# Kernel optimization log

Hardware: AMD Instinct MI355X
Metric: run time of the kernel (lower is better)

Reference implementation:

```python
import jax, jax.numpy as jnp
import numpy as np

DIM = 256
HEADS = 8
W = 64  # window size (1D)
CPB = 512


def setup_inputs() -> dict:
    key = jax.random.key(0)
    ks = jax.random.split(key, 8)
    x = jax.random.normal(ks[0], (4096, W, DIM), dtype=jnp.float32)
    qkv_w = jax.random.normal(ks[1], (3 * DIM, DIM), dtype=jnp.float32) * (1.0 / np.sqrt(DIM))
    q_bias = jnp.zeros((DIM,), dtype=jnp.float32)
    v_bias = jnp.zeros((DIM,), dtype=jnp.float32)
    logit_scale = jnp.full((HEADS, 1, 1), np.log(10.0), dtype=jnp.float32)
    cpb_w1 = jax.random.normal(ks[2], (CPB, 1), dtype=jnp.float32)
    cpb_b1 = jnp.zeros((CPB,), dtype=jnp.float32)
    cpb_w2 = jax.random.normal(ks[3], (HEADS, CPB), dtype=jnp.float32) * (1.0 / np.sqrt(CPB))
    proj_w = jax.random.normal(ks[4], (DIM, DIM), dtype=jnp.float32) * (1.0 / np.sqrt(DIM))
    proj_b = jnp.zeros((DIM,), dtype=jnp.float32)
    return {"x": x, "qkv_w": qkv_w, "q_bias": q_bias, "v_bias": v_bias,
            "logit_scale": logit_scale, "cpb_w1": cpb_w1, "cpb_b1": cpb_b1,
            "cpb_w2": cpb_w2, "proj_w": proj_w, "proj_b": proj_b}


def _rel_coords_table():
    # [2W-1, 1] log-spaced continuous relative coordinates (Swin-v2 CPB input)
    t = jnp.arange(-(W - 1), W, dtype=jnp.float32) / (W - 1) * 8.0
    t = jnp.sign(t) * jnp.log2(jnp.abs(t) + 1.0) / np.log2(8.0)
    return t[:, None]


def _rel_index():
    c = jnp.arange(W)
    return c[:, None] - c[None, :] + (W - 1)  # [W, W] in [0, 2W-2]


def reference(x, qkv_w, q_bias, v_bias, logit_scale, cpb_w1, cpb_b1, cpb_w2, proj_w, proj_b):
    B_, N, C = x.shape
    hd = C // HEADS
    qkv_bias = jnp.concatenate([q_bias, jnp.zeros_like(v_bias), v_bias])
    qkv = x @ qkv_w.T + qkv_bias                                  # [B_, N, 3C]
    qkv = qkv.reshape(B_, N, 3, HEADS, hd).transpose(2, 0, 3, 1, 4)
    q, k, v = qkv[0], qkv[1], qkv[2]                              # [B_, H, N, hd]
    qn = q / jnp.linalg.norm(q, axis=-1, keepdims=True)
    kn = k / jnp.linalg.norm(k, axis=-1, keepdims=True)
    attn = jnp.einsum('bhnd,bhmd->bhnm', qn, kn)
    scale = jnp.exp(jnp.minimum(logit_scale, np.log(1.0 / 0.01)))  # [H,1,1]
    attn = attn * scale[None]
    # CPB relative position bias
    table = jax.nn.relu(_rel_coords_table() @ cpb_w1.T + cpb_b1) @ cpb_w2.T  # [2W-1, H]
    bias = table[_rel_index()]                                    # [W, W, H]
    bias = 16.0 * jax.nn.sigmoid(bias.transpose(2, 0, 1))         # [H, W, W]
    attn = jax.nn.softmax(attn + bias[None], axis=-1)
    out = jnp.einsum('bhnm,bhmd->bhnd', attn, v)
    out = out.transpose(0, 2, 1, 3).reshape(B_, N, C)
    return out @ proj_w.T + proj_b
```

## Files before the change

kernel.cpp:

```cpp
#include <hip/hip_runtime.h>

typedef __attribute__((ext_vector_type(8))) short short8;
typedef __attribute__((ext_vector_type(4))) float f4;

__device__ __forceinline__ float b2f(unsigned short u) {
  union { unsigned int i; float f; } v; v.i = ((unsigned int)u) << 16; return v.f;
}
__device__ __forceinline__ unsigned short f2b(float f) {
  union { float f; unsigned int i; } v; v.f = f;
  unsigned int r = (v.i + 0x7FFFu + ((v.i >> 16) & 1u)) >> 16;
  return (unsigned short)r;
}

template<bool WF32>
__device__ __forceinline__ float ldv(const void* p, int i) {
  if constexpr (WF32) return ((const float*)p)[i];
  else return b2f(((const unsigned short*)p)[i]);
}

template<bool WF32>
__device__ __forceinline__ short8 ld8(const void* p, long idx) {
  short8 r;
  if constexpr (WF32) {
    const float4* f = (const float4*)((const float*)p + idx);
    float4 a = f[0], b = f[1];
    r[0] = (short)f2b(a.x); r[1] = (short)f2b(a.y);
    r[2] = (short)f2b(a.z); r[3] = (short)f2b(a.w);
    r[4] = (short)f2b(b.x); r[5] = (short)f2b(b.y);
    r[6] = (short)f2b(b.z); r[7] = (short)f2b(b.w);
  } else {
    r = *(const short8*)((const unsigned short*)p + idx);
  }
  return r;
}

#define OFF_PROJW 196608
#define OFF_QB    262144
#define OFF_VB    262400
#define OFF_PB    262656
#define OFF_LSC   262912
#define CONV_TOT  262920

__global__ void conv_kernel(const float* __restrict__ qkv_w, const float* __restrict__ proj_w,
                            const float* __restrict__ q_bias, const float* __restrict__ v_bias,
                            const float* __restrict__ proj_b, const float* __restrict__ lsc,
                            unsigned short* __restrict__ wbf) {
  int i = blockIdx.x * 256 + threadIdx.x;
  if (i >= CONV_TOT) return;
  float v;
  if (i < OFF_PROJW)      v = qkv_w[i];
  else if (i < OFF_QB)    v = proj_w[i - OFF_PROJW];
  else if (i < OFF_VB)    v = q_bias[i - OFF_QB];
  else if (i < OFF_PB)    v = v_bias[i - OFF_VB];
  else if (i < OFF_LSC)   v = proj_b[i - OFF_PB];
  else                    v = lsc[i - OFF_LSC];
  wbf[i] = f2b(v);
}

__global__ void cpb_kernel(const float* __restrict__ w1, const float* __restrict__ b1,
                           const float* __restrict__ w2, float* __restrict__ biasv) {
  int p = blockIdx.x * 256 + threadIdx.x;
  if (p >= 127 * 8) return;
  int d = p >> 3, h = p & 7;
  float t = (float)(d - 63) * (8.0f / 63.0f);
  float sgn = (float)((t > 0.f) - (t < 0.f));
  float rc = sgn * log2f(fabsf(t) + 1.f) * (1.f / 3.f);
  float acc = 0.f;
  for (int j = 0; j < 512; ++j) {
    float hj = fmaxf(rc * w1[j] + b1[j], 0.f);
    acc += hj * w2[h * 512 + j];
  }
  biasv[h * 128 + d] = 16.f / (1.f + __expf(-acc));
}

#define XS_S 264
#define QN_S 40
#define VT_S 72
#define PS_S 72
#define OH_S 40

template<bool WF32>
__device__ __forceinline__ void wattn_body(
    const float* x, const void* qkv_w, const void* q_bias, const void* v_bias,
    const void* lsc, const float* biasv, const void* proj_w, const void* proj_b,
    float* out,
    unsigned short* xs, unsigned short* qn, unsigned short* kn,
    unsigned short* vt, unsigned short* Ps, unsigned short* Oh, float* bvs) {
  const int tid = threadIdx.x;
  const int lane = tid & 63;
  const int wv = tid >> 6;
  const int c = lane & 15;
  const int quad = lane >> 4;

  const long b = blockIdx.x;
  const long xbase = b * (64L * 256L);

#pragma unroll
  for (int i = 0; i < 8; ++i) {
    int chunk = tid + 256 * i;
    int row = chunk >> 5;
    int col = (chunk & 31) * 8;
    *(short8*)&xs[row * XS_S + col] = ld8<true>(x, xbase + row * 256 + col);
  }
  for (int i = tid; i < 1024; i += 256) bvs[i] = biasv[i];

  f4 accp[4][4];
#pragma unroll
  for (int i = 0; i < 4; ++i)
#pragma unroll
    for (int j = 0; j < 4; ++j) accp[i][j] = (f4){0.f, 0.f, 0.f, 0.f};

  __syncthreads();

  for (int h = 0; h < 8; ++h) {
    if (wv < 3) {
      f4 acc[4][2];
#pragma unroll
      for (int mt = 0; mt < 4; ++mt)
#pragma unroll
        for (int t = 0; t < 2; ++t) acc[mt][t] = (f4){0.f, 0.f, 0.f, 0.f};

      const long wbase = (long)(wv * 256 + h * 32) * 256L;
#pragma unroll
      for (int k0 = 0; k0 < 256; k0 += 32) {
        short8 a[4], bb[2];
#pragma unroll
        for (int mt = 0; mt < 4; ++mt)
          a[mt] = *(const short8*)&xs[(16 * mt + c) * XS_S + k0 + quad * 8];
#pragma unroll
        for (int t = 0; t < 2; ++t)
          bb[t] = ld8<WF32>(qkv_w, wbase + (long)(16 * t + c) * 256 + k0 + quad * 8);
#pragma unroll
        for (int mt = 0; mt < 4; ++mt)
#pragma unroll
          for (int t = 0; t < 2; ++t)
            acc[mt][t] = __builtin_amdgcn_mfma_f32_16x16x32_bf16(a[mt], bb[t], acc[mt][t], 0, 0, 0);
      }

      if (wv == 0) {
        float qb0 = ldv<WF32>(q_bias, h * 32 + c);
        float qb1 = ldv<WF32>(q_bias, h * 32 + 16 + c);
#pragma unroll
        for (int mt = 0; mt < 4; ++mt)
#pragma unroll
          for (int r = 0; r < 4; ++r) {
            float v0 = acc[mt][0][r] + qb0;
            float v1 = acc[mt][1][r] + qb1;
            float ss = v0 * v0 + v1 * v1;
            ss += __shfl_xor(ss, 1);
            ss += __shfl_xor(ss, 2);
            ss += __shfl_xor(ss, 4);
            ss += __shfl_xor(ss, 8);
            float ri = rsqrtf(ss);
            int m = 16 * mt + quad * 4 + r;
            qn[m * QN_S + c] = f2b(v0 * ri);
            qn[m * QN_S + 16 + c] = f2b(v1 * ri);
          }
      } else if (wv == 1) {
#pragma unroll
        for (int mt = 0; mt < 4; ++mt)
#pragma unroll
          for (int r = 0; r < 4; ++r) {
            float v0 = acc[mt][0][r];
            float v1 = acc[mt][1][r];
            float ss = v0 * v0 + v1 * v1;
            ss += __shfl_xor(ss, 1);
            ss += __shfl_xor(ss, 2);
            ss += __shfl_xor(ss, 4);
            ss += __shfl_xor(ss, 8);
            float ri = rsqrtf(ss);
            int m = 16 * mt + quad * 4 + r;
            kn[m * QN_S + c] = f2b(v0 * ri);
            kn[m * QN_S + 16 + c] = f2b(v1 * ri);
          }
      } else {
        float vb0 = ldv<WF32>(v_bias, h * 32 + c);
        float vb1 = ldv<WF32>(v_bias, h * 32 + 16 + c);
#pragma unroll
        for (int mt = 0; mt < 4; ++mt)
#pragma unroll
          for (int r = 0; r < 4; ++r) {
            int m = 16 * mt + quad * 4 + r;
            vt[c * VT_S + m] = f2b(acc[mt][0][r] + vb0);
            vt[(16 + c) * VT_S + m] = f2b(acc[mt][1][r] + vb1);
          }
      }
    }
    __syncthreads();

    float scale = __expf(fminf(ldv<WF32>(lsc, h), 4.6051702f));

    f4 s[4];
#pragma unroll
    for (int nt = 0; nt < 4; ++nt) s[nt] = (f4){0.f, 0.f, 0.f, 0.f};
    short8 aq = *(const short8*)&qn[(16 * wv + c) * QN_S + quad * 8];
#pragma unroll
    for (int nt = 0; nt < 4; ++nt) {
      short8 bk = *(const short8*)&kn[(16 * nt + c) * QN_S + quad * 8];
      s[nt] = __builtin_amdgcn_mfma_f32_16x16x32_bf16(aq, bk, s[nt], 0, 0, 0);
    }

#pragma unroll
    for (int r = 0; r < 4; ++r) {
      int m = 16 * wv + quad * 4 + r;
      float l[4];
#pragma unroll
      for (int nt = 0; nt < 4; ++nt) {
        int n = 16 * nt + c;
        l[nt] = s[nt][r] * scale + bvs[h * 128 + (m - n + 63)];
      }
      float mx = fmaxf(fmaxf(l[0], l[1]), fmaxf(l[2], l[3]));
      mx = fmaxf(mx, __shfl_xor(mx, 1));
      mx = fmaxf(mx, __shfl_xor(mx, 2));
      mx = fmaxf(mx, __shfl_xor(mx, 4));
      mx = fmaxf(mx, __shfl_xor(mx, 8));
      float p[4];
      float sum = 0.f;
#pragma unroll
      for (int nt = 0; nt < 4; ++nt) { p[nt] = __expf(l[nt] - mx); sum += p[nt]; }
      sum += __shfl_xor(sum, 1);
      sum += __shfl_xor(sum, 2);
      sum += __shfl_xor(sum, 4);
      sum += __shfl_xor(sum, 8);
      float inv = 1.f / sum;
#pragma unroll
      for (int nt = 0; nt < 4; ++nt)
        Ps[m * PS_S + 16 * nt + c] = f2b(p[nt] * inv);
    }

    f4 o[2];
    o[0] = (f4){0.f, 0.f, 0.f, 0.f};
    o[1] = (f4){0.f, 0.f, 0.f, 0.f};
#pragma unroll
    for (int k0 = 0; k0 < 64; k0 += 32) {
      short8 ap = *(const short8*)&Ps[(16 * wv + c) * PS_S + k0 + quad * 8];
#pragma unroll
      for (int t = 0; t < 2; ++t) {
        short8 bvv = *(const short8*)&vt[(16 * t + c) * VT_S + k0 + quad * 8];
        o[t] = __builtin_amdgcn_mfma_f32_16x16x32_bf16(ap, bvv, o[t], 0, 0, 0);
      }
    }
#pragma unroll
    for (int t = 0; t < 2; ++t)
#pragma unroll
      for (int r = 0; r < 4; ++r) {
        int m = 16 * wv + quad * 4 + r;
        Oh[m * OH_S + 16 * t + c] = f2b(o[t][r]);
      }
    __syncthreads();

    {
      const long pbase = (long)(64 * wv) * 256L + h * 32;
      short8 ao[4], bp[4];
#pragma unroll
      for (int mt = 0; mt < 4; ++mt)
        ao[mt] = *(const short8*)&Oh[(16 * mt + c) * OH_S + quad * 8];
#pragma unroll
      for (int nt = 0; nt < 4; ++nt)
        bp[nt] = ld8<WF32>(proj_w, pbase + (long)(16 * nt + c) * 256 + quad * 8);
#pragma unroll
      for (int mt = 0; mt < 4; ++mt)
#pragma unroll
        for (int nt = 0; nt < 4; ++nt)
          accp[mt][nt] = __builtin_amdgcn_mfma_f32_16x16x32_bf16(ao[mt], bp[nt], accp[mt][nt], 0, 0, 0);
    }
    __syncthreads();
  }

  float pb[4];
#pragma unroll
  for (int nt = 0; nt < 4; ++nt) pb[nt] = ldv<WF32>(proj_b, 64 * wv + 16 * nt + c);
  float* og = out + b * 16384L;
#pragma unroll
  for (int mt = 0; mt < 4; ++mt)
#pragma unroll
    for (int r = 0; r < 4; ++r) {
      int m = 16 * mt + quad * 4 + r;
#pragma unroll
      for (int nt = 0; nt < 4; ++nt)
        og[m * 256 + 64 * wv + 16 * nt + c] = accp[mt][nt][r] + pb[nt];
    }
}

template<bool WF32>
__launch_bounds__(256, 2)
__global__ void wattn_kernel(const float* __restrict__ x, const void* __restrict__ qkv_w,
                             const void* __restrict__ q_bias, const void* __restrict__ v_bias,
                             const void* __restrict__ lsc, const float* __restrict__ biasv,
                             const void* __restrict__ proj_w, const void* __restrict__ proj_b,
                             float* __restrict__ out) {
  __shared__ __align__(16) unsigned short xs[64 * XS_S];
  __shared__ __align__(16) unsigned short qn[64 * QN_S];
  __shared__ __align__(16) unsigned short kn[64 * QN_S];
  __shared__ __align__(16) unsigned short vt[32 * VT_S];
  __shared__ __align__(16) unsigned short Ps[64 * PS_S];
  __shared__ __align__(16) unsigned short Oh[64 * OH_S];
  __shared__ float bvs[8 * 128];

  wattn_body<WF32>(x, qkv_w, q_bias, v_bias, lsc, biasv, proj_w, proj_b, out,
                   xs, qn, kn, vt, Ps, Oh, bvs);
}

extern "C" void kernel_launch(void* const* d_in, const int* in_sizes, int n_in,
                              void* d_out, int out_size, void* d_ws, size_t ws_size,
                              hipStream_t stream) {
  const float* x      = (const float*)d_in[0];
  const float* qkv_w  = (const float*)d_in[1];
  const float* q_bias = (const float*)d_in[2];
  const float* v_bias = (const float*)d_in[3];
  const float* lsc    = (const float*)d_in[4];
  const float* cpb_w1 = (const float*)d_in[5];
  const float* cpb_b1 = (const float*)d_in[6];
  const float* cpb_w2 = (const float*)d_in[7];
  const float* proj_w = (const float*)d_in[8];
  const float* proj_b = (const float*)d_in[9];
  float* out = (float*)d_out;

  float* biasv = (float*)d_ws;
  unsigned short* wbf = (unsigned short*)((char*)d_ws + 4096);

  int nwin = in_sizes[0] / (64 * 256);
  size_t need = 4096 + (size_t)CONV_TOT * 2 + 64;

  cpb_kernel<<<4, 256, 0, stream>>>(cpb_w1, cpb_b1, cpb_w2, biasv);

  if (ws_size >= need) {
    conv_kernel<<<(CONV_TOT + 255) / 256, 256, 0, stream>>>(
        qkv_w, proj_w, q_bias, v_bias, proj_b, lsc, wbf);
    wattn_kernel<false><<<nwin, 256, 0, stream>>>(
        x, wbf, wbf + OFF_QB, wbf + OFF_VB, wbf + OFF_LSC, biasv,
        wbf + OFF_PROJW, wbf + OFF_PB, out);
  } else {
    wattn_kernel<true><<<nwin, 256, 0, stream>>>(
        x, qkv_w, q_bias, v_bias, lsc, biasv, proj_w, proj_b, out);
  }
}
```

Baseline: 852.3 us.

## Process four heads per phase with 512-thread blocks in window attention

The fused window-attention kernel grows from 4 to 8 waves per block and handles heads in two groups of four instead of looping over 8 heads one at a time. In the old loop one wave sat idle during the QKV GEMM and there were three barriers per head. Now all 8 waves share the QKV projection tile for 128 columns of q/k/v, each wave pair computes attention for one head, and the projection GEMM has a K depth of 128 per phase. This cuts barriers and wave idleness and raises MFMA work per load, at the cost of more LDS (wider qn/kn/vt/Ps buffers) and possibly lower occupancy.

```diff
diff --git a/kernel.cpp b/kernel.cpp
--- a/kernel.cpp
+++ b/kernel.cpp
@@ -74,216 +74,13 @@
 }
 
 #define XS_S 264
-#define QN_S 40
+#define QN_S 136
 #define VT_S 72
 #define PS_S 72
-#define OH_S 40
+#define OH_S 136
 
 template<bool WF32>
-__device__ __forceinline__ void wattn_body(
-    const float* x, const void* qkv_w, const void* q_bias, const void* v_bias,
-    const void* lsc, const float* biasv, const void* proj_w, const void* proj_b,
-    float* out,
-    unsigned short* xs, unsigned short* qn, unsigned short* kn,
-    unsigned short* vt, unsigned short* Ps, unsigned short* Oh, float* bvs) {
-  const int tid = threadIdx.x;
-  const int lane = tid & 63;
-  const int wv = tid >> 6;
-  const int c = lane & 15;
-  const int quad = lane >> 4;
-
-  const long b = blockIdx.x;
-  const long xbase = b * (64L * 256L);
-
-#pragma unroll
-  for (int i = 0; i < 8; ++i) {
-    int chunk = tid + 256 * i;
-    int row = chunk >> 5;
-    int col = (chunk & 31) * 8;
-    *(short8*)&xs[row * XS_S + col] = ld8<true>(x, xbase + row * 256 + col);
-  }
-  for (int i = tid; i < 1024; i += 256) bvs[i] = biasv[i];
-
-  f4 accp[4][4];
-#pragma unroll
-  for (int i = 0; i < 4; ++i)
-#pragma unroll
-    for (int j = 0; j < 4; ++j) accp[i][j] = (f4){0.f, 0.f, 0.f, 0.f};
-
-  __syncthreads();
-
-  for (int h = 0; h < 8; ++h) {
-    if (wv < 3) {
-      f4 acc[4][2];
-#pragma unroll
-      for (int mt = 0; mt < 4; ++mt)
-#pragma unroll
-        for (int t = 0; t < 2; ++t) acc[mt][t] = (f4){0.f, 0.f, 0.f, 0.f};
-
-      const long wbase = (long)(wv * 256 + h * 32) * 256L;
-#pragma unroll
-      for (int k0 = 0; k0 < 256; k0 += 32) {
-        short8 a[4], bb[2];
-#pragma unroll
-        for (int mt = 0; mt < 4; ++mt)
-          a[mt] = *(const short8*)&xs[(16 * mt + c) * XS_S + k0 + quad * 8];
-#pragma unroll
-        for (int t = 0; t < 2; ++t)
-          bb[t] = ld8<WF32>(qkv_w, wbase + (long)(16 * t + c) * 256 + k0 + quad * 8);
-#pragma unroll
-        for (int mt = 0; mt < 4; ++mt)
-#pragma unroll
-          for (int t = 0; t < 2; ++t)
-            acc[mt][t] = __builtin_amdgcn_mfma_f32_16x16x32_bf16(a[mt], bb[t], acc[mt][t], 0, 0, 0);
-      }
-
-      if (wv == 0) {
-        float qb0 = ldv<WF32>(q_bias, h * 32 + c);
-        float qb1 = ldv<WF32>(q_bias, h * 32 + 16 + c);
-#pragma unroll
-        for (int mt = 0; mt < 4; ++mt)
-#pragma unroll
-          for (int r = 0; r < 4; ++r) {
-            float v0 = acc[mt][0][r] + qb0;
-            float v1 = acc[mt][1][r] + qb1;
-            float ss = v0 * v0 + v1 * v1;
-            ss += __shfl_xor(ss, 1);
-            ss += __shfl_xor(ss, 2);
-            ss += __shfl_xor(ss, 4);
-            ss += __shfl_xor(ss, 8);
-            float ri = rsqrtf(ss);
-            int m = 16 * mt + quad * 4 + r;
-            qn[m * QN_S + c] = f2b(v0 * ri);
-            qn[m * QN_S + 16 + c] = f2b(v1 * ri);
-          }
-      } else if (wv == 1) {
-#pragma unroll
-        for (int mt = 0; mt < 4; ++mt)
-#pragma unroll
-          for (int r = 0; r < 4; ++r) {
-            float v0 = acc[mt][0][r];
-            float v1 = acc[mt][1][r];
-            float ss = v0 * v0 + v1 * v1;
-            ss += __shfl_xor(ss, 1);
-            ss += __shfl_xor(ss, 2);
-            ss += __shfl_xor(ss, 4);
-            ss += __shfl_xor(ss, 8);
-            float ri = rsqrtf(ss);
-            int m = 16 * mt + quad * 4 + r;
-            kn[m * QN_S + c] = f2b(v0 * ri);
-            kn[m * QN_S + 16 + c] = f2b(v1 * ri);
-          }
-      } else {
-        float vb0 = ldv<WF32>(v_bias, h * 32 + c);
-        float vb1 = ldv<WF32>(v_bias, h * 32 + 16 + c);
-#pragma unroll
-        for (int mt = 0; mt < 4; ++mt)
-#pragma unroll
-          for (int r = 0; r < 4; ++r) {
-            int m = 16 * mt + quad * 4 + r;
-            vt[c * VT_S + m] = f2b(acc[mt][0][r] + vb0);
-            vt[(16 + c) * VT_S + m] = f2b(acc[mt][1][r] + vb1);
-          }
-      }
-    }
-    __syncthreads();
-
-    float scale = __expf(fminf(ldv<WF32>(lsc, h), 4.6051702f));
-
-    f4 s[4];
-#pragma unroll
-    for (int nt = 0; nt < 4; ++nt) s[nt] = (f4){0.f, 0.f, 0.f, 0.f};
-    short8 aq = *(const short8*)&qn[(16 * wv + c) * QN_S + quad * 8];
-#pragma unroll
-    for (int nt = 0; nt < 4; ++nt) {
-      short8 bk = *(const short8*)&kn[(16 * nt + c) * QN_S + quad * 8];
-      s[nt] = __builtin_amdgcn_mfma_f32_16x16x32_bf16(aq, bk, s[nt], 0, 0, 0);
-    }
-
-#pragma unroll
-    for (int r = 0; r < 4; ++r) {
-      int m = 16 * wv + quad * 4 + r;
-      float l[4];
-#pragma unroll
-      for (int nt = 0; nt < 4; ++nt) {
-        int n = 16 * nt + c;
-        l[nt] = s[nt][r] * scale + bvs[h * 128 + (m - n + 63)];
-      }
-      float mx = fmaxf(fmaxf(l[0], l[1]), fmaxf(l[2], l[3]));
-      mx = fmaxf(mx, __shfl_xor(mx, 1));
-      mx = fmaxf(mx, __shfl_xor(mx, 2));
-      mx = fmaxf(mx, __shfl_xor(mx, 4));
-      mx = fmaxf(mx, __shfl_xor(mx, 8));
-      float p[4];
-      float sum = 0.f;
-#pragma unroll
-      for (int nt = 0; nt < 4; ++nt) { p[nt] = __expf(l[nt] - mx); sum += p[nt]; }
-      sum += __shfl_xor(sum, 1);
-      sum += __shfl_xor(sum, 2);
-      sum += __shfl_xor(sum, 4);
-      sum += __shfl_xor(sum, 8);
-      float inv = 1.f / sum;
-#pragma unroll
-      for (int nt = 0; nt < 4; ++nt)
-        Ps[m * PS_S + 16 * nt + c] = f2b(p[nt] * inv);
-    }
-
-    f4 o[2];
-    o[0] = (f4){0.f, 0.f, 0.f, 0.f};
-    o[1] = (f4){0.f, 0.f, 0.f, 0.f};
-#pragma unroll
-    for (int k0 = 0; k0 < 64; k0 += 32) {
-      short8 ap = *(const short8*)&Ps[(16 * wv + c) * PS_S + k0 + quad * 8];
-#pragma unroll
-      for (int t = 0; t < 2; ++t) {
-        short8 bvv = *(const short8*)&vt[(16 * t + c) * VT_S + k0 + quad * 8];
-        o[t] = __builtin_amdgcn_mfma_f32_16x16x32_bf16(ap, bvv, o[t], 0, 0, 0);
-      }
-    }
-#pragma unroll
-    for (int t = 0; t < 2; ++t)
-#pragma unroll
-      for (int r = 0; r < 4; ++r) {
-        int m = 16 * wv + quad * 4 + r;
-        Oh[m * OH_S + 16 * t + c] = f2b(o[t][r]);
-      }
-    __syncthreads();
-
-    {
-      const long pbase = (long)(64 * wv) * 256L + h * 32;
-      short8 ao[4], bp[4];
-#pragma unroll
-      for (int mt = 0; mt < 4; ++mt)
-        ao[mt] = *(const short8*)&Oh[(16 * mt + c) * OH_S + quad * 8];
-#pragma unroll
-      for (int nt = 0; nt < 4; ++nt)
-        bp[nt] = ld8<WF32>(proj_w, pbase + (long)(16 * nt + c) * 256 + quad * 8);
-#pragma unroll
-      for (int mt = 0; mt < 4; ++mt)
-#pragma unroll
-        for (int nt = 0; nt < 4; ++nt)
-          accp[mt][nt] = __builtin_amdgcn_mfma_f32_16x16x32_bf16(ao[mt], bp[nt], accp[mt][nt], 0, 0, 0);
-    }
-    __syncthreads();
-  }
-
-  float pb[4];
-#pragma unroll
-  for (int nt = 0; nt < 4; ++nt) pb[nt] = ldv<WF32>(proj_b, 64 * wv + 16 * nt + c);
-  float* og = out + b * 16384L;
-#pragma unroll
-  for (int mt = 0; mt < 4; ++mt)
-#pragma unroll
-    for (int r = 0; r < 4; ++r) {
-      int m = 16 * mt + quad * 4 + r;
-#pragma unroll
-      for (int nt = 0; nt < 4; ++nt)
-        og[m * 256 + 64 * wv + 16 * nt + c] = accp[mt][nt][r] + pb[nt];
-    }
-}
-
-template<bool WF32>
-__launch_bounds__(256, 2)
+__launch_bounds__(512, 2)
 __global__ void wattn_kernel(const float* __restrict__ x, const void* __restrict__ qkv_w,
                              const void* __restrict__ q_bias, const void* __restrict__ v_bias,
                              const void* __restrict__ lsc, const float* __restrict__ biasv,
@@ -292,13 +89,239 @@
   __shared__ __align__(16) unsigned short xs[64 * XS_S];
   __shared__ __align__(16) unsigned short qn[64 * QN_S];
   __shared__ __align__(16) unsigned short kn[64 * QN_S];
-  __shared__ __align__(16) unsigned short vt[32 * VT_S];
-  __shared__ __align__(16) unsigned short Ps[64 * PS_S];
-  __shared__ __align__(16) unsigned short Oh[64 * OH_S];
+  __shared__ __align__(16) unsigned short vt[128 * VT_S];
+  __shared__ __align__(16) unsigned short Ps[4 * 64 * PS_S];
   __shared__ float bvs[8 * 128];
-
-  wattn_body<WF32>(x, qkv_w, q_bias, v_bias, lsc, biasv, proj_w, proj_b, out,
-                   xs, qn, kn, vt, Ps, Oh, bvs);
+  unsigned short* const Oh = Ps;
+
+  const int tid = threadIdx.x;
+  const int lane = tid & 63;
+  const int wv = tid >> 6;
+  const int c = lane & 15;
+  const int quad = lane >> 4;
+
+  const long b = blockIdx.x;
+  const long xbase = b * (64L * 256L);
+
+#pragma unroll
+  for (int i = 0; i < 4; ++i) {
+    int chunk = tid + 512 * i;
+    int row = chunk >> 5;
+    int col = (chunk & 31) * 8;
+    *(short8*)&xs[row * XS_S + col] = ld8<true>(x, xbase + row * 256 + col);
+  }
+#pragma unroll
+  for (int i = tid; i < 1024; i += 512) bvs[i] = biasv[i];
+
+  f4 accp[4][2];
+#pragma unroll
+  for (int i = 0; i < 4; ++i)
+#pragma unroll
+    for (int j = 0; j < 2; ++j) accp[i][j] = (f4){0.f, 0.f, 0.f, 0.f};
+
+  __syncthreads();
+
+  for (int it = 0; it < 2; ++it) {
+    {
+      const int r2 = wv & 1;
+      const int c4 = wv >> 1;
+      f4 acc[2][6];
+#pragma unroll
+      for (int mt = 0; mt < 2; ++mt)
+#pragma unroll
+        for (int nt = 0; nt < 6; ++nt) acc[mt][nt] = (f4){0.f, 0.f, 0.f, 0.f};
+
+      long wbase[6];
+#pragma unroll
+      for (int nt = 0; nt < 6; ++nt) {
+        int cc = 96 * c4 + 16 * nt;
+        int part = cc >> 7;
+        int lc = cc & 127;
+        wbase[nt] = (long)(part * 256 + it * 128 + lc + c) * 256L;
+      }
+      const int arow0 = (32 * r2 + c) * XS_S;
+      const int arow1 = (32 * r2 + 16 + c) * XS_S;
+#pragma unroll
+      for (int k0 = 0; k0 < 256; k0 += 32) {
+        short8 a0 = *(const short8*)&xs[arow0 + k0 + quad * 8];
+        short8 a1 = *(const short8*)&xs[arow1 + k0 + quad * 8];
+        short8 bb[6];
+#pragma unroll
+        for (int nt = 0; nt < 6; ++nt)
+          bb[nt] = ld8<WF32>(qkv_w, wbase[nt] + k0 + quad * 8);
+#pragma unroll
+        for (int nt = 0; nt < 6; ++nt) {
+          acc[0][nt] = __builtin_amdgcn_mfma_f32_16x16x32_bf16(a0, bb[nt], acc[0][nt], 0, 0, 0);
+          acc[1][nt] = __builtin_amdgcn_mfma_f32_16x16x32_bf16(a1, bb[nt], acc[1][nt], 0, 0, 0);
+        }
+      }
+#pragma unroll
+      for (int j = 0; j < 3; ++j) {
+        const int cc = 96 * c4 + 32 * j;
+        const int part = cc >> 7;
+        const int lc = cc & 127;
+        if (part == 0) {
+          float qb0 = ldv<WF32>(q_bias, it * 128 + lc + c);
+          float qb1 = ldv<WF32>(q_bias, it * 128 + lc + 16 + c);
+#pragma unroll
+          for (int mt = 0; mt < 2; ++mt)
+#pragma unroll
+            for (int r = 0; r < 4; ++r) {
+              float v0 = acc[mt][2 * j][r] + qb0;
+              float v1 = acc[mt][2 * j + 1][r] + qb1;
+              float ss = v0 * v0 + v1 * v1;
+              ss += __shfl_xor(ss, 1);
+              ss += __shfl_xor(ss, 2);
+              ss += __shfl_xor(ss, 4);
+              ss += __shfl_xor(ss, 8);
+              float ri = rsqrtf(ss);
+              int m = 32 * r2 + 16 * mt + quad * 4 + r;
+              qn[m * QN_S + lc + c] = f2b(v0 * ri);
+              qn[m * QN_S + lc + 16 + c] = f2b(v1 * ri);
+            }
+        } else if (part == 1) {
+#pragma unroll
+          for (int mt = 0; mt < 2; ++mt)
+#pragma unroll
+            for (int r = 0; r < 4; ++r) {
+              float v0 = acc[mt][2 * j][r];
+              float v1 = acc[mt][2 * j + 1][r];
+              float ss = v0 * v0 + v1 * v1;
+              ss += __shfl_xor(ss, 1);
+              ss += __shfl_xor(ss, 2);
+              ss += __shfl_xor(ss, 4);
+              ss += __shfl_xor(ss, 8);
+              float ri = rsqrtf(ss);
+              int m = 32 * r2 + 16 * mt + quad * 4 + r;
+              kn[m * QN_S + lc + c] = f2b(v0 * ri);
+              kn[m * QN_S + lc + 16 + c] = f2b(v1 * ri);
+            }
+        } else {
+          float vb0 = ldv<WF32>(v_bias, it * 128 + lc + c);
+          float vb1 = ldv<WF32>(v_bias, it * 128 + lc + 16 + c);
+#pragma unroll
+          for (int mt = 0; mt < 2; ++mt)
+#pragma unroll
+            for (int r = 0; r < 4; ++r) {
+              int m = 32 * r2 + 16 * mt + quad * 4 + r;
+              vt[(lc + c) * VT_S + m] = f2b(acc[mt][2 * j][r] + vb0);
+              vt[(lc + 16 + c) * VT_S + m] = f2b(acc[mt][2 * j + 1][r] + vb1);
+            }
+        }
+      }
+    }
+    __syncthreads();
+
+    {
+      const int hl = wv >> 1;
+      const int rs = wv & 1;
+      const int h = 4 * it + hl;
+      const float scale = __expf(fminf(ldv<WF32>(lsc, h), 4.6051702f));
+
+      f4 s[2][4];
+#pragma unroll
+      for (int mt = 0; mt < 2; ++mt)
+#pragma unroll
+        for (int nt = 0; nt < 4; ++nt) s[mt][nt] = (f4){0.f, 0.f, 0.f, 0.f};
+
+      short8 aq0 = *(const short8*)&qn[(32 * rs + c) * QN_S + 32 * hl + quad * 8];
+      short8 aq1 = *(const short8*)&qn[(32 * rs + 16 + c) * QN_S + 32 * hl + quad * 8];
+#pragma unroll
+      for (int nt = 0; nt < 4; ++nt) {
+        short8 bk = *(const short8*)&kn[(16 * nt + c) * QN_S + 32 * hl + quad * 8];
+        s[0][nt] = __builtin_amdgcn_mfma_f32_16x16x32_bf16(aq0, bk, s[0][nt], 0, 0, 0);
+        s[1][nt] = __builtin_amdgcn_mfma_f32_16x16x32_bf16(aq1, bk, s[1][nt], 0, 0, 0);
+      }
+
+      const float* bvh = bvs + h * 128 + 63;
+#pragma unroll
+      for (int mt = 0; mt < 2; ++mt)
+#pragma unroll
+        for (int r = 0; r < 4; ++r) {
+          const int m = 32 * rs + 16 * mt + quad * 4 + r;
+          float l[4];
+#pragma unroll
+          for (int nt = 0; nt < 4; ++nt)
+            l[nt] = s[mt][nt][r] * scale + bvh[m - 16 * nt - c];
+          float mx = fmaxf(fmaxf(l[0], l[1]), fmaxf(l[2], l[3]));
+          mx = fmaxf(mx, __shfl_xor(mx, 1));
+          mx = fmaxf(mx, __shfl_xor(mx, 2));
+          mx = fmaxf(mx, __shfl_xor(mx, 4));
+          mx = fmaxf(mx, __shfl_xor(mx, 8));
+          float p[4];
+          float sum = 0.f;
+#pragma unroll
+          for (int nt = 0; nt < 4; ++nt) { p[nt] = __expf(l[nt] - mx); sum += p[nt]; }
+          sum += __shfl_xor(sum, 1);
+          sum += __shfl_xor(sum, 2);
+          sum += __shfl_xor(sum, 4);
+          sum += __shfl_xor(sum, 8);
+          float inv = 1.f / sum;
+#pragma unroll
+          for (int nt = 0; nt < 4; ++nt)
+            Ps[(hl * 64 + m) * PS_S + 16 * nt + c] = f2b(p[nt] * inv);
+        }
+
+      f4 o[2][2];
+#pragma unroll
+      for (int mt = 0; mt < 2; ++mt)
+#pragma unroll
+        for (int t = 0; t < 2; ++t) o[mt][t] = (f4){0.f, 0.f, 0.f, 0.f};
+#pragma unroll
+      for (int k0 = 0; k0 < 64; k0 += 32) {
+        short8 ap0 = *(const short8*)&Ps[(hl * 64 + 32 * rs + c) * PS_S + k0 + quad * 8];
+        short8 ap1 = *(const short8*)&Ps[(hl * 64 + 32 * rs + 16 + c) * PS_S + k0 + quad * 8];
+#pragma unroll
+        for (int t = 0; t < 2; ++t) {
+          short8 bvv = *(const short8*)&vt[(32 * hl + 16 * t + c) * VT_S + k0 + quad * 8];
+          o[0][t] = __builtin_amdgcn_mfma_f32_16x16x32_bf16(ap0, bvv, o[0][t], 0, 0, 0);
+          o[1][t] = __builtin_amdgcn_mfma_f32_16x16x32_bf16(ap1, bvv, o[1][t], 0, 0, 0);
+        }
+      }
+      __syncthreads();
+#pragma unroll
+      for (int mt = 0; mt < 2; ++mt)
+#pragma unroll
+        for (int t = 0; t < 2; ++t)
+#pragma unroll
+          for (int r = 0; r < 4; ++r) {
+            int m = 32 * rs + 16 * mt + quad * 4 + r;
+            Oh[m * OH_S + 32 * hl + 16 * t + c] = f2b(o[mt][t][r]);
+          }
+    }
+    __syncthreads();
+
+    {
+#pragma unroll
+      for (int k0 = 0; k0 < 128; k0 += 32) {
+        short8 ao[4];
+#pragma unroll
+        for (int mt = 0; mt < 4; ++mt)
+          ao[mt] = *(const short8*)&Oh[(16 * mt + c) * OH_S + k0 + quad * 8];
+        short8 bp[2];
+#pragma unroll
+        for (int nt = 0; nt < 2; ++nt)
+          bp[nt] = ld8<WF32>(proj_w, (long)(32 * wv + 16 * nt + c) * 256L + it * 128 + k0 + quad * 8);
+#pragma unroll
+        for (int mt = 0; mt < 4; ++mt)
+#pragma unroll
+          for (int nt = 0; nt < 2; ++nt)
+            accp[mt][nt] = __builtin_amdgcn_mfma_f32_16x16x32_bf16(ao[mt], bp[nt], accp[mt][nt], 0, 0, 0);
+      }
+    }
+  }
+
+  float pb0 = ldv<WF32>(proj_b, 32 * wv + c);
+  float pb1 = ldv<WF32>(proj_b, 32 * wv + 16 + c);
+  float* og = out + b * 16384L;
+#pragma unroll
+  for (int mt = 0; mt < 4; ++mt)
+#pragma unroll
+    for (int r = 0; r < 4; ++r) {
+      int m = 16 * mt + quad * 4 + r;
+      og[m * 256 + 32 * wv + c] = accp[mt][0][r] + pb0;
+      og[m * 256 + 32 * wv + 16 + c] = accp[mt][1][r] + pb1;
+    }
 }
 
 extern "C" void kernel_launch(void* const* d_in, const int* in_sizes, int n_in,
@@ -327,11 +350,11 @@
   if (ws_size >= need) {
     conv_kernel<<<(CONV_TOT + 255) / 256, 256, 0, stream>>>(
         qkv_w, proj_w, q_bias, v_bias, proj_b, lsc, wbf);
-    wattn_kernel<false><<<nwin, 256, 0, stream>>>(
+    wattn_kernel<false><<<nwin, 512, 0, stream>>>(
         x, wbf, wbf + OFF_QB, wbf + OFF_VB, wbf + OFF_LSC, biasv,
         wbf + OFF_PROJW, wbf + OFF_PB, out);
   } else {
-    wattn_kernel<true><<<nwin, 256, 0, stream>>>(
+    wattn_kernel<true><<<nwin, 512, 0, stream>>>(
         x, qkv_w, q_bias, v_bias, lsc, biasv, proj_w, proj_b, out);
   }
 }
```

After: 1.032 ms. +21.1%, slower.

## Keep x rows in registers per wave and split QKV by rows

Applied to the files above, without the earlier changes.

The kernel no longer stages the x window in LDS. Each wave keeps its own 16 rows of x as MFMA A-fragments in registers and computes Q, K and V for those rows, replacing the old split where three waves each did one of Q, K or V for all rows. The Oh buffer is dropped by writing the attention output back into Ps, one trailing barrier per head is removed, and launch bounds are raised to 3 blocks per CU. This cuts LDS use and synchronisation to allow higher occupancy. In exchange every wave now fetches all qkv weight tiles from global memory or L2, and register pressure rises.

```diff
diff --git a/kernel.cpp b/kernel.cpp
--- a/kernel.cpp
+++ b/kernel.cpp
@@ -73,19 +73,23 @@
   biasv[h * 128 + d] = 16.f / (1.f + __expf(-acc));
 }
 
-#define XS_S 264
 #define QN_S 40
 #define VT_S 72
 #define PS_S 72
-#define OH_S 40
 
 template<bool WF32>
-__device__ __forceinline__ void wattn_body(
-    const float* x, const void* qkv_w, const void* q_bias, const void* v_bias,
-    const void* lsc, const float* biasv, const void* proj_w, const void* proj_b,
-    float* out,
-    unsigned short* xs, unsigned short* qn, unsigned short* kn,
-    unsigned short* vt, unsigned short* Ps, unsigned short* Oh, float* bvs) {
+__launch_bounds__(256, 3)
+__global__ void wattn_kernel(const float* __restrict__ x, const void* __restrict__ qkv_w,
+                             const void* __restrict__ q_bias, const void* __restrict__ v_bias,
+                             const void* __restrict__ lsc, const float* __restrict__ biasv,
+                             const void* __restrict__ proj_w, const void* __restrict__ proj_b,
+                             float* __restrict__ out) {
+  __shared__ __align__(16) unsigned short qn[64 * QN_S];
+  __shared__ __align__(16) unsigned short kn[64 * QN_S];
+  __shared__ __align__(16) unsigned short vt[32 * VT_S];
+  __shared__ __align__(16) unsigned short Ps[64 * PS_S];
+  __shared__ float bvs[8 * 128];
+
   const int tid = threadIdx.x;
   const int lane = tid & 63;
   const int wv = tid >> 6;
@@ -95,13 +99,11 @@
   const long b = blockIdx.x;
   const long xbase = b * (64L * 256L);
 
-#pragma unroll
-  for (int i = 0; i < 8; ++i) {
-    int chunk = tid + 256 * i;
-    int row = chunk >> 5;
-    int col = (chunk & 31) * 8;
-    *(short8*)&xs[row * XS_S + col] = ld8<true>(x, xbase + row * 256 + col);
-  }
+  short8 af[8];
+#pragma unroll
+  for (int kt = 0; kt < 8; ++kt)
+    af[kt] = ld8<true>(x, xbase + (long)(16 * wv + c) * 256 + kt * 32 + quad * 8);
+
   for (int i = tid; i < 1024; i += 256) bvs[i] = biasv[i];
 
   f4 accp[4][4];
@@ -113,140 +115,130 @@
   __syncthreads();
 
   for (int h = 0; h < 8; ++h) {
-    if (wv < 3) {
-      f4 acc[4][2];
-#pragma unroll
-      for (int mt = 0; mt < 4; ++mt)
-#pragma unroll
-        for (int t = 0; t < 2; ++t) acc[mt][t] = (f4){0.f, 0.f, 0.f, 0.f};
-
-      const long wbase = (long)(wv * 256 + h * 32) * 256L;
-#pragma unroll
-      for (int k0 = 0; k0 < 256; k0 += 32) {
-        short8 a[4], bb[2];
-#pragma unroll
-        for (int mt = 0; mt < 4; ++mt)
-          a[mt] = *(const short8*)&xs[(16 * mt + c) * XS_S + k0 + quad * 8];
-#pragma unroll
-        for (int t = 0; t < 2; ++t)
-          bb[t] = ld8<WF32>(qkv_w, wbase + (long)(16 * t + c) * 256 + k0 + quad * 8);
-#pragma unroll
-        for (int mt = 0; mt < 4; ++mt)
+    {
+      f4 acc[3][2];
+#pragma unroll
+      for (int p = 0; p < 3; ++p)
+#pragma unroll
+        for (int t = 0; t < 2; ++t) acc[p][t] = (f4){0.f, 0.f, 0.f, 0.f};
+
+#pragma unroll
+      for (int kt = 0; kt < 8; ++kt) {
+        short8 bb[6];
+#pragma unroll
+        for (int p = 0; p < 3; ++p)
 #pragma unroll
           for (int t = 0; t < 2; ++t)
-            acc[mt][t] = __builtin_amdgcn_mfma_f32_16x16x32_bf16(a[mt], bb[t], acc[mt][t], 0, 0, 0);
-      }
-
-      if (wv == 0) {
-        float qb0 = ldv<WF32>(q_bias, h * 32 + c);
-        float qb1 = ldv<WF32>(q_bias, h * 32 + 16 + c);
-#pragma unroll
-        for (int mt = 0; mt < 4; ++mt)
-#pragma unroll
-          for (int r = 0; r < 4; ++r) {
-            float v0 = acc[mt][0][r] + qb0;
-            float v1 = acc[mt][1][r] + qb1;
-            float ss = v0 * v0 + v1 * v1;
-            ss += __shfl_xor(ss, 1);
-            ss += __shfl_xor(ss, 2);
-            ss += __shfl_xor(ss, 4);
-            ss += __shfl_xor(ss, 8);
-            float ri = rsqrtf(ss);
-            int m = 16 * mt + quad * 4 + r;
-            qn[m * QN_S + c] = f2b(v0 * ri);
-            qn[m * QN_S + 16 + c] = f2b(v1 * ri);
-          }
-      } else if (wv == 1) {
-#pragma unroll
-        for (int mt = 0; mt < 4; ++mt)
-#pragma unroll
-          for (int r = 0; r < 4; ++r) {
-            float v0 = acc[mt][0][r];
-            float v1 = acc[mt][1][r];
-            float ss = v0 * v0 + v1 * v1;
-            ss += __shfl_xor(ss, 1);
-            ss += __shfl_xor(ss, 2);
-            ss += __shfl_xor(ss, 4);
-            ss += __shfl_xor(ss, 8);
-            float ri = rsqrtf(ss);
-            int m = 16 * mt + quad * 4 + r;
-            kn[m * QN_S + c] = f2b(v0 * ri);
-            kn[m * QN_S + 16 + c] = f2b(v1 * ri);
-          }
-      } else {
-        float vb0 = ldv<WF32>(v_bias, h * 32 + c);
-        float vb1 = ldv<WF32>(v_bias, h * 32 + 16 + c);
-#pragma unroll
-        for (int mt = 0; mt < 4; ++mt)
-#pragma unroll
-          for (int r = 0; r < 4; ++r) {
-            int m = 16 * mt + quad * 4 + r;
-            vt[c * VT_S + m] = f2b(acc[mt][0][r] + vb0);
-            vt[(16 + c) * VT_S + m] = f2b(acc[mt][1][r] + vb1);
-          }
+            bb[p * 2 + t] = ld8<WF32>(qkv_w,
+                (long)(p * 256 + h * 32 + 16 * t + c) * 256 + kt * 32 + quad * 8);
+#pragma unroll
+        for (int p = 0; p < 3; ++p)
+#pragma unroll
+          for (int t = 0; t < 2; ++t)
+            acc[p][t] = __builtin_amdgcn_mfma_f32_16x16x32_bf16(af[kt], bb[p * 2 + t], acc[p][t], 0, 0, 0);
+      }
+
+      float qb0 = ldv<WF32>(q_bias, h * 32 + c);
+      float qb1 = ldv<WF32>(q_bias, h * 32 + 16 + c);
+#pragma unroll
+      for (int r = 0; r < 4; ++r) {
+        float v0 = acc[0][0][r] + qb0;
+        float v1 = acc[0][1][r] + qb1;
+        float ss = v0 * v0 + v1 * v1;
+        ss += __shfl_xor(ss, 1);
+        ss += __shfl_xor(ss, 2);
+        ss += __shfl_xor(ss, 4);
+        ss += __shfl_xor(ss, 8);
+        float ri = rsqrtf(ss);
+        int m = 16 * wv + quad * 4 + r;
+        qn[m * QN_S + c] = f2b(v0 * ri);
+        qn[m * QN_S + 16 + c] = f2b(v1 * ri);
+      }
+#pragma unroll
+      for (int r = 0; r < 4; ++r) {
+        float v0 = acc[1][0][r];
+        float v1 = acc[1][1][r];
+        float ss = v0 * v0 + v1 * v1;
+        ss += __shfl_xor(ss, 1);
+        ss += __shfl_xor(ss, 2);
+        ss += __shfl_xor(ss, 4);
+        ss += __shfl_xor(ss, 8);
+        float ri = rsqrtf(ss);
+        int m = 16 * wv + quad * 4 + r;
+        kn[m * QN_S + c] = f2b(v0 * ri);
+        kn[m * QN_S + 16 + c] = f2b(v1 * ri);
+      }
+      float vb0 = ldv<WF32>(v_bias, h * 32 + c);
+      float vb1 = ldv<WF32>(v_bias, h * 32 + 16 + c);
+#pragma unroll
+      for (int r = 0; r < 4; ++r) {
+        int m = 16 * wv + quad * 4 + r;
+        vt[c * VT_S + m] = f2b(acc[2][0][r] + vb0);
+        vt[(16 + c) * VT_S + m] = f2b(acc[2][1][r] + vb1);
       }
     }
     __syncthreads();
 
-    float scale = __expf(fminf(ldv<WF32>(lsc, h), 4.6051702f));
-
-    f4 s[4];
-#pragma unroll
-    for (int nt = 0; nt < 4; ++nt) s[nt] = (f4){0.f, 0.f, 0.f, 0.f};
-    short8 aq = *(const short8*)&qn[(16 * wv + c) * QN_S + quad * 8];
-#pragma unroll
-    for (int nt = 0; nt < 4; ++nt) {
-      short8 bk = *(const short8*)&kn[(16 * nt + c) * QN_S + quad * 8];
-      s[nt] = __builtin_amdgcn_mfma_f32_16x16x32_bf16(aq, bk, s[nt], 0, 0, 0);
-    }
-
-#pragma unroll
-    for (int r = 0; r < 4; ++r) {
-      int m = 16 * wv + quad * 4 + r;
-      float l[4];
+    {
+      float scale = __expf(fminf(ldv<WF32>(lsc, h), 4.6051702f));
+
+      f4 s[4];
+#pragma unroll
+      for (int nt = 0; nt < 4; ++nt) s[nt] = (f4){0.f, 0.f, 0.f, 0.f};
+      short8 aq = *(const short8*)&qn[(16 * wv + c) * QN_S + quad * 8];
 #pragma unroll
       for (int nt = 0; nt < 4; ++nt) {
-        int n = 16 * nt + c;
-        l[nt] = s[nt][r] * scale + bvs[h * 128 + (m - n + 63)];
-      }
-      float mx = fmaxf(fmaxf(l[0], l[1]), fmaxf(l[2], l[3]));
-      mx = fmaxf(mx, __shfl_xor(mx, 1));
-      mx = fmaxf(mx, __shfl_xor(mx, 2));
-      mx = fmaxf(mx, __shfl_xor(mx, 4));
-      mx = fmaxf(mx, __shfl_xor(mx, 8));
-      float p[4];
-      float sum = 0.f;
-#pragma unroll
-      for (int nt = 0; nt < 4; ++nt) { p[nt] = __expf(l[nt] - mx); sum += p[nt]; }
-      sum += __shfl_xor(sum, 1);
-      sum += __shfl_xor(sum, 2);
-      sum += __shfl_xor(sum, 4);
-      sum += __shfl_xor(sum, 8);
-      float inv = 1.f / sum;
-#pragma unroll
-      for (int nt = 0; nt < 4; ++nt)
-        Ps[m * PS_S + 16 * nt + c] = f2b(p[nt] * inv);
-    }
-
-    f4 o[2];
-    o[0] = (f4){0.f, 0.f, 0.f, 0.f};
-    o[1] = (f4){0.f, 0.f, 0.f, 0.f};
-#pragma unroll
-    for (int k0 = 0; k0 < 64; k0 += 32) {
-      short8 ap = *(const short8*)&Ps[(16 * wv + c) * PS_S + k0 + quad * 8];
-#pragma unroll
-      for (int t = 0; t < 2; ++t) {
-        short8 bvv = *(const short8*)&vt[(16 * t + c) * VT_S + k0 + quad * 8];
-        o[t] = __builtin_amdgcn_mfma_f32_16x16x32_bf16(ap, bvv, o[t], 0, 0, 0);
-      }
-    }
-#pragma unroll
-    for (int t = 0; t < 2; ++t)
+        short8 bk = *(const short8*)&kn[(16 * nt + c) * QN_S + quad * 8];
+        s[nt] = __builtin_amdgcn_mfma_f32_16x16x32_bf16(aq, bk, s[nt], 0, 0, 0);
+      }
+
+      const float* bvh = bvs + h * 128 + 63;
 #pragma unroll
       for (int r = 0; r < 4; ++r) {
         int m = 16 * wv + quad * 4 + r;
-        Oh[m * OH_S + 16 * t + c] = f2b(o[t][r]);
-      }
+        float l[4];
+#pragma unroll
+        for (int nt = 0; nt < 4; ++nt)
+          l[nt] = s[nt][r] * scale + bvh[m - 16 * nt - c];
+        float mx = fmaxf(fmaxf(l[0], l[1]), fmaxf(l[2], l[3]));
+        mx = fmaxf(mx, __shfl_xor(mx, 1));
+        mx = fmaxf(mx, __shfl_xor(mx, 2));
+        mx = fmaxf(mx, __shfl_xor(mx, 4));
+        mx = fmaxf(mx, __shfl_xor(mx, 8));
+        float p[4];
+        float sum = 0.f;
+#pragma unroll
+        for (int nt = 0; nt < 4; ++nt) { p[nt] = __expf(l[nt] - mx); sum += p[nt]; }
+        sum += __shfl_xor(sum, 1);
+        sum += __shfl_xor(sum, 2);
+        sum += __shfl_xor(sum, 4);
+        sum += __shfl_xor(sum, 8);
+        float inv = 1.f / sum;
+#pragma unroll
+        for (int nt = 0; nt < 4; ++nt)
+          Ps[m * PS_S + 16 * nt + c] = f2b(p[nt] * inv);
+      }
+
+      f4 o[2];
+      o[0] = (f4){0.f, 0.f, 0.f, 0.f};
+      o[1] = (f4){0.f, 0.f, 0.f, 0.f};
+#pragma unroll
+      for (int k0 = 0; k0 < 64; k0 += 32) {
+        short8 ap = *(const short8*)&Ps[(16 * wv + c) * PS_S + k0 + quad * 8];
+#pragma unroll
+        for (int t = 0; t < 2; ++t) {
+          short8 bvv = *(const short8*)&vt[(16 * t + c) * VT_S + k0 + quad * 8];
+          o[t] = __builtin_amdgcn_mfma_f32_16x16x32_bf16(ap, bvv, o[t], 0, 0, 0);
+        }
+      }
+#pragma unroll
+      for (int t = 0; t < 2; ++t)
+#pragma unroll
+        for (int r = 0; r < 4; ++r) {
+          int m = 16 * wv + quad * 4 + r;
+          Ps[m * PS_S + 16 * t + c] = f2b(o[t][r]);
+        }
+    }
     __syncthreads();
 
     {
@@ -254,7 +246,7 @@
       short8 ao[4], bp[4];
 #pragma unroll
       for (int mt = 0; mt < 4; ++mt)
-        ao[mt] = *(const short8*)&Oh[(16 * mt + c) * OH_S + quad * 8];
+        ao[mt] = *(const short8*)&Ps[(16 * mt + c) * PS_S + quad * 8];
 #pragma unroll
       for (int nt = 0; nt < 4; ++nt)
         bp[nt] = ld8<WF32>(proj_w, pbase + (long)(16 * nt + c) * 256 + quad * 8);
@@ -264,7 +256,6 @@
         for (int nt = 0; nt < 4; ++nt)
           accp[mt][nt] = __builtin_amdgcn_mfma_f32_16x16x32_bf16(ao[mt], bp[nt], accp[mt][nt], 0, 0, 0);
     }
-    __syncthreads();
   }
 
   float pb[4];
@@ -280,25 +271,6 @@
       for (int nt = 0; nt < 4; ++nt)
         og[m * 256 + 64 * wv + 16 * nt + c] = accp[mt][nt][r] + pb[nt];
     }
-}
-
-template<bool WF32>
-__launch_bounds__(256, 2)
-__global__ void wattn_kernel(const float* __restrict__ x, const void* __restrict__ qkv_w,
-                             const void* __restrict__ q_bias, const void* __restrict__ v_bias,
-                             const void* __restrict__ lsc, const float* __restrict__ biasv,
-                             const void* __restrict__ proj_w, const void* __restrict__ proj_b,
-                             float* __restrict__ out) {
-  __shared__ __align__(16) unsigned short xs[64 * XS_S];
-  __shared__ __align__(16) unsigned short qn[64 * QN_S];
-  __shared__ __align__(16) unsigned short kn[64 * QN_S];
-  __shared__ __align__(16) unsigned short vt[32 * VT_S];
-  __shared__ __align__(16) unsigned short Ps[64 * PS_S];
-  __shared__ __align__(16) unsigned short Oh[64 * OH_S];
-  __shared__ float bvs[8 * 128];
-
-  wattn_body<WF32>(x, qkv_w, q_bias, v_bias, lsc, biasv, proj_w, proj_b, out,
-                   xs, qn, kn, vt, Ps, Oh, bvs);
 }
 
 extern "C" void kernel_launch(void* const* d_in, const int* in_sizes, int n_in,
```

Measured after the change: 1.867 ms. 119% more time.

## Defer per-head output projection into next head's QKV phase and rebalance waves

Applied to the files above, without the earlier changes.

Waves 0-1 now compute Q and K, while waves 2-3 split the V projection between them. Waves 2-3 also run the output projection for the previous head, overlapping it with the QKV GEMMs. This removes one block-wide barrier per head and the separate Oh shared buffer, since the attention output is written back into Ps. The aim is to balance MFMA work across all four waves instead of leaving one idle. The cost is that waves 2-3 hold a 4x8 accumulator tile, which raises register pressure, and the final head's projection becomes a tail step.

```diff
diff --git a/kernel.cpp b/kernel.cpp
--- a/kernel.cpp
+++ b/kernel.cpp
@@ -77,15 +77,21 @@
 #define QN_S 40
 #define VT_S 72
 #define PS_S 72
-#define OH_S 40
 
 template<bool WF32>
-__device__ __forceinline__ void wattn_body(
-    const float* x, const void* qkv_w, const void* q_bias, const void* v_bias,
-    const void* lsc, const float* biasv, const void* proj_w, const void* proj_b,
-    float* out,
-    unsigned short* xs, unsigned short* qn, unsigned short* kn,
-    unsigned short* vt, unsigned short* Ps, unsigned short* Oh, float* bvs) {
+__launch_bounds__(256, 2)
+__global__ void wattn_kernel(const float* __restrict__ x, const void* __restrict__ qkv_w,
+                             const void* __restrict__ q_bias, const void* __restrict__ v_bias,
+                             const void* __restrict__ lsc, const float* __restrict__ biasv,
+                             const void* __restrict__ proj_w, const void* __restrict__ proj_b,
+                             float* __restrict__ out) {
+  __shared__ __align__(16) unsigned short xs[64 * XS_S];
+  __shared__ __align__(16) unsigned short qn[64 * QN_S];
+  __shared__ __align__(16) unsigned short kn[64 * QN_S];
+  __shared__ __align__(16) unsigned short vt[32 * VT_S];
+  __shared__ __align__(16) unsigned short Ps[64 * PS_S];
+  __shared__ float bvs[8 * 128];
+
   const int tid = threadIdx.x;
   const int lane = tid & 63;
   const int wv = tid >> 6;
@@ -104,16 +110,18 @@
   }
   for (int i = tid; i < 1024; i += 256) bvs[i] = biasv[i];
 
-  f4 accp[4][4];
-#pragma unroll
-  for (int i = 0; i < 4; ++i)
-#pragma unroll
-    for (int j = 0; j < 4; ++j) accp[i][j] = (f4){0.f, 0.f, 0.f, 0.f};
+  f4 accp[4][8];
+  if (wv >= 2) {
+#pragma unroll
+    for (int i = 0; i < 4; ++i)
+#pragma unroll
+      for (int j = 0; j < 8; ++j) accp[i][j] = (f4){0.f, 0.f, 0.f, 0.f};
+  }
 
   __syncthreads();
 
   for (int h = 0; h < 8; ++h) {
-    if (wv < 3) {
+    if (wv < 2) {
       f4 acc[4][2];
 #pragma unroll
       for (int mt = 0; mt < 4; ++mt)
@@ -156,7 +164,7 @@
             qn[m * QN_S + c] = f2b(v0 * ri);
             qn[m * QN_S + 16 + c] = f2b(v1 * ri);
           }
-      } else if (wv == 1) {
+      } else {
 #pragma unroll
         for (int mt = 0; mt < 4; ++mt)
 #pragma unroll
@@ -173,132 +181,143 @@
             kn[m * QN_S + c] = f2b(v0 * ri);
             kn[m * QN_S + 16 + c] = f2b(v1 * ri);
           }
-      } else {
-        float vb0 = ldv<WF32>(v_bias, h * 32 + c);
-        float vb1 = ldv<WF32>(v_bias, h * 32 + 16 + c);
-#pragma unroll
-        for (int mt = 0; mt < 4; ++mt)
-#pragma unroll
-          for (int r = 0; r < 4; ++r) {
-            int m = 16 * mt + quad * 4 + r;
-            vt[c * VT_S + m] = f2b(acc[mt][0][r] + vb0);
-            vt[(16 + c) * VT_S + m] = f2b(acc[mt][1][r] + vb1);
-          }
+      }
+    } else {
+      const int half = wv & 1;
+      f4 acc[4];
+#pragma unroll
+      for (int mt = 0; mt < 4; ++mt) acc[mt] = (f4){0.f, 0.f, 0.f, 0.f};
+
+      const long wbase = (long)(512 + h * 32 + 16 * half + c) * 256L;
+#pragma unroll
+      for (int k0 = 0; k0 < 256; k0 += 32) {
+        short8 bb = ld8<WF32>(qkv_w, wbase + k0 + quad * 8);
+#pragma unroll
+        for (int mt = 0; mt < 4; ++mt) {
+          short8 a = *(const short8*)&xs[(16 * mt + c) * XS_S + k0 + quad * 8];
+          acc[mt] = __builtin_amdgcn_mfma_f32_16x16x32_bf16(a, bb, acc[mt], 0, 0, 0);
+        }
+      }
+
+      float vb = ldv<WF32>(v_bias, h * 32 + 16 * half + c);
+#pragma unroll
+      for (int mt = 0; mt < 4; ++mt)
+#pragma unroll
+        for (int r = 0; r < 4; ++r) {
+          int m = 16 * mt + quad * 4 + r;
+          vt[(16 * half + c) * VT_S + m] = f2b(acc[mt][r] + vb);
+        }
+
+      if (h > 0) {
+        const int hp = h - 1;
+        short8 ao[4];
+#pragma unroll
+        for (int mt = 0; mt < 4; ++mt)
+          ao[mt] = *(const short8*)&Ps[(16 * mt + c) * PS_S + quad * 8];
+#pragma unroll
+        for (int nt = 0; nt < 8; ++nt) {
+          short8 bp = ld8<WF32>(proj_w,
+              (long)(128 * half + 16 * nt + c) * 256L + hp * 32 + quad * 8);
+#pragma unroll
+          for (int mt = 0; mt < 4; ++mt)
+            accp[mt][nt] = __builtin_amdgcn_mfma_f32_16x16x32_bf16(ao[mt], bp, accp[mt][nt], 0, 0, 0);
+        }
       }
     }
     __syncthreads();
 
-    float scale = __expf(fminf(ldv<WF32>(lsc, h), 4.6051702f));
-
-    f4 s[4];
-#pragma unroll
-    for (int nt = 0; nt < 4; ++nt) s[nt] = (f4){0.f, 0.f, 0.f, 0.f};
-    short8 aq = *(const short8*)&qn[(16 * wv + c) * QN_S + quad * 8];
-#pragma unroll
-    for (int nt = 0; nt < 4; ++nt) {
-      short8 bk = *(const short8*)&kn[(16 * nt + c) * QN_S + quad * 8];
-      s[nt] = __builtin_amdgcn_mfma_f32_16x16x32_bf16(aq, bk, s[nt], 0, 0, 0);
-    }
-
-#pragma unroll
-    for (int r = 0; r < 4; ++r) {
-      int m = 16 * wv + quad * 4 + r;
-      float l[4];
+    {
+      float scale = __expf(fminf(ldv<WF32>(lsc, h), 4.6051702f));
+
+      f4 s[4];
+#pragma unroll
+      for (int nt = 0; nt < 4; ++nt) s[nt] = (f4){0.f, 0.f, 0.f, 0.f};
+      short8 aq = *(const short8*)&qn[(16 * wv + c) * QN_S + quad * 8];
 #pragma unroll
       for (int nt = 0; nt < 4; ++nt) {
-        int n = 16 * nt + c;
-        l[nt] = s[nt][r] * scale + bvs[h * 128 + (m - n + 63)];
-      }
-      float mx = fmaxf(fmaxf(l[0], l[1]), fmaxf(l[2], l[3]));
-      mx = fmaxf(mx, __shfl_xor(mx, 1));
-      mx = fmaxf(mx, __shfl_xor(mx, 2));
-      mx = fmaxf(mx, __shfl_xor(mx, 4));
-      mx = fmaxf(mx, __shfl_xor(mx, 8));
-      float p[4];
-      float sum = 0.f;
-#pragma unroll
-      for (int nt = 0; nt < 4; ++nt) { p[nt] = __expf(l[nt] - mx); sum += p[nt]; }
-      sum += __shfl_xor(sum, 1);
-      sum += __shfl_xor(sum, 2);
-      sum += __shfl_xor(sum, 4);
-      sum += __shfl_xor(sum, 8);
-      float inv = 1.f / sum;
-#pragma unroll
-      for (int nt = 0; nt < 4; ++nt)
-        Ps[m * PS_S + 16 * nt + c] = f2b(p[nt] * inv);
-    }
-
-    f4 o[2];
-    o[0] = (f4){0.f, 0.f, 0.f, 0.f};
-    o[1] = (f4){0.f, 0.f, 0.f, 0.f};
-#pragma unroll
-    for (int k0 = 0; k0 < 64; k0 += 32) {
-      short8 ap = *(const short8*)&Ps[(16 * wv + c) * PS_S + k0 + quad * 8];
-#pragma unroll
-      for (int t = 0; t < 2; ++t) {
-        short8 bvv = *(const short8*)&vt[(16 * t + c) * VT_S + k0 + quad * 8];
-        o[t] = __builtin_amdgcn_mfma_f32_16x16x32_bf16(ap, bvv, o[t], 0, 0, 0);
-      }
-    }
-#pragma unroll
-    for (int t = 0; t < 2; ++t)
+        short8 bk = *(const short8*)&kn[(16 * nt + c) * QN_S + quad * 8];
+        s[nt] = __builtin_amdgcn_mfma_f32_16x16x32_bf16(aq, bk, s[nt], 0, 0, 0);
+      }
+
+      const float* bvh = bvs + h * 128 + 63;
 #pragma unroll
       for (int r = 0; r < 4; ++r) {
         int m = 16 * wv + quad * 4 + r;
-        Oh[m * OH_S + 16 * t + c] = f2b(o[t][r]);
-      }
-    __syncthreads();
-
-    {
-      const long pbase = (long)(64 * wv) * 256L + h * 32;
-      short8 ao[4], bp[4];
-#pragma unroll
-      for (int mt = 0; mt < 4; ++mt)
-        ao[mt] = *(const short8*)&Oh[(16 * mt + c) * OH_S + quad * 8];
-#pragma unroll
-      for (int nt = 0; nt < 4; ++nt)
-        bp[nt] = ld8<WF32>(proj_w, pbase + (long)(16 * nt + c) * 256 + quad * 8);
-#pragma unroll
-      for (int mt = 0; mt < 4; ++mt)
+        float l[4];
 #pragma unroll
         for (int nt = 0; nt < 4; ++nt)
-          accp[mt][nt] = __builtin_amdgcn_mfma_f32_16x16x32_bf16(ao[mt], bp[nt], accp[mt][nt], 0, 0, 0);
+          l[nt] = s[nt][r] * scale + bvh[m - 16 * nt - c];
+        float mx = fmaxf(fmaxf(l[0], l[1]), fmaxf(l[2], l[3]));
+        mx = fmaxf(mx, __shfl_xor(mx, 1));
+        mx = fmaxf(mx, __shfl_xor(mx, 2));
+        mx = fmaxf(mx, __shfl_xor(mx, 4));
+        mx = fmaxf(mx, __shfl_xor(mx, 8));
+        float p[4];
+        float sum = 0.f;
+#pragma unroll
+        for (int nt = 0; nt < 4; ++nt) { p[nt] = __expf(l[nt] - mx); sum += p[nt]; }
+        sum += __shfl_xor(sum, 1);
+        sum += __shfl_xor(sum, 2);
+        sum += __shfl_xor(sum, 4);
+        sum += __shfl_xor(sum, 8);
+        float inv = 1.f / sum;
+#pragma unroll
+        for (int nt = 0; nt < 4; ++nt)
+          Ps[m * PS_S + 16 * nt + c] = f2b(p[nt] * inv);
+      }
+
+      f4 o[2];
+      o[0] = (f4){0.f, 0.f, 0.f, 0.f};
+      o[1] = (f4){0.f, 0.f, 0.f, 0.f};
+#pragma unroll
+      for (int k0 = 0; k0 < 64; k0 += 32) {
+        short8 ap = *(const short8*)&Ps[(16 * wv + c) * PS_S + k0 + quad * 8];
+#pragma unroll
+        for (int t = 0; t < 2; ++t) {
+          short8 bvv = *(const short8*)&vt[(16 * t + c) * VT_S + k0 + quad * 8];
+          o[t] = __builtin_amdgcn_mfma_f32_16x16x32_bf16(ap, bvv, o[t], 0, 0, 0);
+        }
+      }
+#pragma unroll
+      for (int t = 0; t < 2; ++t)
+#pragma unroll
+        for (int r = 0; r < 4; ++r) {
+          int m = 16 * wv + quad * 4 + r;
+          Ps[m * PS_S + 16 * t + c] = f2b(o[t][r]);
+        }
     }
     __syncthreads();
   }
 
-  float pb[4];
-#pragma unroll
-  for (int nt = 0; nt < 4; ++nt) pb[nt] = ldv<WF32>(proj_b, 64 * wv + 16 * nt + c);
-  float* og = out + b * 16384L;
-#pragma unroll
-  for (int mt = 0; mt < 4; ++mt)
-#pragma unroll
-    for (int r = 0; r < 4; ++r) {
-      int m = 16 * mt + quad * 4 + r;
-#pragma unroll
-      for (int nt = 0; nt < 4; ++nt)
-        og[m * 256 + 64 * wv + 16 * nt + c] = accp[mt][nt][r] + pb[nt];
+  if (wv >= 2) {
+    const int half = wv & 1;
+    short8 ao[4];
+#pragma unroll
+    for (int mt = 0; mt < 4; ++mt)
+      ao[mt] = *(const short8*)&Ps[(16 * mt + c) * PS_S + quad * 8];
+#pragma unroll
+    for (int nt = 0; nt < 8; ++nt) {
+      short8 bp = ld8<WF32>(proj_w,
+          (long)(128 * half + 16 * nt + c) * 256L + 7 * 32 + quad * 8);
+#pragma unroll
+      for (int mt = 0; mt < 4; ++mt)
+        accp[mt][nt] = __builtin_amdgcn_mfma_f32_16x16x32_bf16(ao[mt], bp, accp[mt][nt], 0, 0, 0);
     }
-}
-
-template<bool WF32>
-__launch_bounds__(256, 2)
-__global__ void wattn_kernel(const float* __restrict__ x, const void* __restrict__ qkv_w,
-                             const void* __restrict__ q_bias, const void* __restrict__ v_bias,
-                             const void* __restrict__ lsc, const float* __restrict__ biasv,
-                             const void* __restrict__ proj_w, const void* __restrict__ proj_b,
-                             float* __restrict__ out) {
-  __shared__ __align__(16) unsigned short xs[64 * XS_S];
-  __shared__ __align__(16) unsigned short qn[64 * QN_S];
-  __shared__ __align__(16) unsigned short kn[64 * QN_S];
-  __shared__ __align__(16) unsigned short vt[32 * VT_S];
-  __shared__ __align__(16) unsigned short Ps[64 * PS_S];
-  __shared__ __align__(16) unsigned short Oh[64 * OH_S];
-  __shared__ float bvs[8 * 128];
-
-  wattn_body<WF32>(x, qkv_w, q_bias, v_bias, lsc, biasv, proj_w, proj_b, out,
-                   xs, qn, kn, vt, Ps, Oh, bvs);
+
+    float pb[8];
+#pragma unroll
+    for (int nt = 0; nt < 8; ++nt) pb[nt] = ldv<WF32>(proj_b, 128 * half + 16 * nt + c);
+    float* og = out + b * 16384L;
+#pragma unroll
+    for (int mt = 0; mt < 4; ++mt)
+#pragma unroll
+      for (int r = 0; r < 4; ++r) {
+        int m = 16 * mt + quad * 4 + r;
+#pragma unroll
+        for (int nt = 0; nt < 8; ++nt)
+          og[m * 256 + 128 * half + 16 * nt + c] = accp[mt][nt][r] + pb[nt];
+      }
+  }
 }
 
 extern "C" void kernel_launch(void* const* d_in, const int* in_sizes, int n_in,
```

Measured after the change: 801.0 us. 1.06x faster.
